# Kernel tuning notes

Measured on AMD Instinct MI355X. Metric: run time of the kernel, lower is better.

## Reference

```python
import jax, jax.numpy as jnp
import numpy as np

SEQ_LEN, BZ, D_IN = 512, 64, 1024
HIDDEN, D_OUT, NUM_LANG = 256, 1024, 16


def setup_inputs() -> dict:
    key = jax.random.key(0)
    ks = jax.random.split(key, 6)
    x = jax.random.normal(ks[0], (SEQ_LEN, BZ, D_IN), dtype=jnp.float32)
    lang_ids = jax.random.randint(ks[1], (BZ,), 0, NUM_LANG, dtype=jnp.int64)
    # Per-language 2-layer MLP params, stacked over the language axis.
    # Stored as [in, out] so y = x @ W + b (same math as torch Linear's x @ W.T + b).
    s1 = 1.0 / np.sqrt(D_IN)
    s2 = 1.0 / np.sqrt(HIDDEN)
    W1 = jax.random.uniform(ks[2], (NUM_LANG, D_IN, HIDDEN), jnp.float32, -s1, s1)
    b1 = jax.random.uniform(ks[3], (NUM_LANG, HIDDEN), jnp.float32, -s1, s1)
    W2 = jax.random.uniform(ks[4], (NUM_LANG, HIDDEN, D_OUT), jnp.float32, -s2, s2)
    b2 = jax.random.uniform(ks[5], (NUM_LANG, D_OUT), jnp.float32, -s2, s2)
    return {"x": x, "lang_ids": lang_ids, "W1": W1, "b1": b1, "W2": W2, "b2": b2}


def reference(x, lang_ids, W1, b1, W2, b2):
    # Gather each batch element's expert weights, then do batched GEMMs.
    # Equivalent to the torch loop (dispatch -> per-expert MLP -> combine),
    # without redundant gather/scatter passes.
    W1g = W1[lang_ids]            # [bz, d_in, hidden]
    b1g = b1[lang_ids]            # [bz, hidden]
    W2g = W2[lang_ids]            # [bz, hidden, d_out]
    b2g = b2[lang_ids]            # [bz, d_out]
    h = jnp.einsum('sbd,bdh->sbh', x, W1g) + b1g[None, :, :]
    h = jax.nn.relu(h)
    y = jnp.einsum('sbh,bho->sbo', h, W2g) + b2g[None, :, :]
    return y
```

## Files before the change

kernel.cpp:

```cpp
#include <hip/hip_runtime.h>

#define SEQ 512
#define BZ  64
#define DIN 1024
#define HID 256
#define DOUT 1024
#define NLANG 16

typedef __attribute__((ext_vector_type(8))) __bf16 bf16x8;
typedef __attribute__((ext_vector_type(4))) float f32x4;

__device__ __forceinline__ unsigned short f2bf(float f) {
    return __builtin_bit_cast(unsigned short, (__bf16)f);
}
__device__ __forceinline__ unsigned int f2bf_pack(float lo, float hi) {
    return (unsigned int)f2bf(lo) | ((unsigned int)f2bf(hi) << 16);
}

template<int K, int N>
__global__ __launch_bounds__(256)
void prep_frags(const float* __restrict__ src, unsigned short* __restrict__ dst) {
    constexpr int K32 = K / 32, N16 = N / 16;
    const int gid = blockIdx.x * 256 + threadIdx.x;
    const int l   = gid & 63;
    const int f   = gid >> 6;
    const int k32 = f & (K32 - 1);
    const int n16 = (f / K32) & (N16 - 1);
    const int lid = f / (K32 * N16);
    const float* s = src + ((long)lid * K + k32 * 32 + (l >> 4) * 8) * N + n16 * 16 + (l & 15);
    unsigned short o[8];
#pragma unroll
    for (int j = 0; j < 8; ++j) o[j] = f2bf(s[(long)j * N]);
    uint4 v;
    v.x = (unsigned int)o[0] | ((unsigned int)o[1] << 16);
    v.y = (unsigned int)o[2] | ((unsigned int)o[3] << 16);
    v.z = (unsigned int)o[4] | ((unsigned int)o[5] << 16);
    v.w = (unsigned int)o[6] | ((unsigned int)o[7] << 16);
    *(uint4*)(dst + (long)gid * 8) = v;
}

__global__ __launch_bounds__(256, 2)
void fused_mlp(const float* __restrict__ x,
               const unsigned short* __restrict__ W1f,
               const float* __restrict__ b1,
               const unsigned short* __restrict__ W2f,
               const float* __restrict__ b2,
               const int* __restrict__ lang,
               float* __restrict__ y) {
    __shared__ unsigned short sA[2][64 * 64];
    __shared__ unsigned short sH[64 * 256];

    const int b  = blockIdx.x;
    const int st = blockIdx.y;
    const int t  = threadIdx.x;
    const int l  = t & 63;
    const int w  = t >> 6;
    const int lid = lang[b];
    const int s0  = st * 64;
    const long xbase = (long)s0 * BZ * DIN + (long)b * DIN;

    const f32x4 z4 = {0.f, 0.f, 0.f, 0.f};

    f32x4 acc1[4][4];
#pragma unroll
    for (int mi = 0; mi < 4; ++mi)
#pragma unroll
        for (int ni = 0; ni < 4; ++ni) acc1[mi][ni] = z4;

    float4 xr[4];
#define LOADX(KT)                                                                 \
    {                                                                             \
        _Pragma("unroll")                                                         \
        for (int j = 0; j < 4; ++j) {                                             \
            int u = t + 256 * j, m = u >> 4, c4 = u & 15;                         \
            xr[j] = *(const float4*)(x + xbase + (long)m * (BZ * DIN) + (KT) * 64 + c4 * 4); \
        }                                                                         \
    }
#define WRITEX(BUF)                                                               \
    {                                                                             \
        char* cA = (char*)sA[BUF];                                                \
        _Pragma("unroll")                                                         \
        for (int j = 0; j < 4; ++j) {                                             \
            int u = t + 256 * j, m = u >> 4, c4 = u & 15;                         \
            uint2 p;                                                              \
            p.x = f2bf_pack(xr[j].x, xr[j].y);                                    \
            p.y = f2bf_pack(xr[j].z, xr[j].w);                                    \
            *(uint2*)(cA + (((m * 128) + c4 * 8) ^ ((m & 7) << 4))) = p;          \
        }                                                                         \
    }

    LOADX(0);
    WRITEX(0);
    __syncthreads();

    const unsigned short* w1p = W1f + (((long)lid * 16 + w * 4) * 32) * 512 + (long)l * 8;

    for (int kt = 0; kt < 16; ++kt) {
        const int cur = kt & 1;
        if (kt < 15) LOADX(kt + 1);

        bf16x8 bv[2][4];
#pragma unroll
        for (int ks = 0; ks < 2; ++ks)
#pragma unroll
            for (int ni = 0; ni < 4; ++ni)
                bv[ks][ni] = __builtin_bit_cast(bf16x8,
                    *(const uint4*)(w1p + (long)ni * 16384 + (kt * 2 + ks) * 512));

        char* cA = (char*)sA[cur];
#pragma unroll
        for (int ks = 0; ks < 2; ++ks) {
            bf16x8 av[4];
#pragma unroll
            for (int mi = 0; mi < 4; ++mi) {
                int row = mi * 16 + (l & 15);
                int ch  = ks * 4 + (l >> 4);
                av[mi] = __builtin_bit_cast(bf16x8,
                    *(const uint4*)(cA + row * 128 + ((ch ^ (row & 7)) << 4)));
            }
#pragma unroll
            for (int mi = 0; mi < 4; ++mi)
#pragma unroll
                for (int ni = 0; ni < 4; ++ni)
                    acc1[mi][ni] = __builtin_amdgcn_mfma_f32_16x16x32_bf16(
                        av[mi], bv[ks][ni], acc1[mi][ni], 0, 0, 0);
        }

        if (kt < 15) WRITEX(cur ^ 1);
        __syncthreads();
    }

    {
        float bvv[4];
#pragma unroll
        for (int ni = 0; ni < 4; ++ni)
            bvv[ni] = b1[lid * HID + w * 64 + ni * 16 + (l & 15)];
        char* cH = (char*)sH;
#pragma unroll
        for (int mi = 0; mi < 4; ++mi)
#pragma unroll
            for (int r = 0; r < 4; ++r) {
                int row = mi * 16 + (l >> 4) * 4 + r;
#pragma unroll
                for (int ni = 0; ni < 4; ++ni) {
                    int col = w * 64 + ni * 16 + (l & 15);
                    float v = acc1[mi][ni][r] + bvv[ni];
                    v = v > 0.f ? v : 0.f;
                    *(unsigned short*)(cH + row * 512 + (((col >> 3) ^ (row & 7)) << 4)
                                       + (col & 7) * 2) = f2bf(v);
                }
            }
    }
    __syncthreads();

    bf16x8 a2[4][8];
    {
        char* cH = (char*)sH;
#pragma unroll
        for (int mi = 0; mi < 4; ++mi)
#pragma unroll
            for (int ks = 0; ks < 8; ++ks) {
                int row = mi * 16 + (l & 15);
                int ch  = ks * 4 + (l >> 4);
                a2[mi][ks] = __builtin_bit_cast(bf16x8,
                    *(const uint4*)(cH + row * 512 + ((ch ^ (row & 7)) << 4)));
            }
    }

    const unsigned short* w2p = W2f + (((long)lid * 64 + w * 16) * 8) * 512 + (long)l * 8;

#pragma unroll 1
    for (int nc = 0; nc < 4; ++nc) {
        f32x4 acc[4][4];
#pragma unroll
        for (int mi = 0; mi < 4; ++mi)
#pragma unroll
            for (int ni = 0; ni < 4; ++ni) acc[mi][ni] = z4;

        const unsigned short* wp = w2p + (long)nc * 4 * 4096;

        bf16x8 pv[2][4];
#pragma unroll
        for (int ni = 0; ni < 4; ++ni)
            pv[0][ni] = __builtin_bit_cast(bf16x8, *(const uint4*)(wp + (long)ni * 4096));
#pragma unroll
        for (int ks = 0; ks < 8; ++ks) {
            const int cb = ks & 1;
            if (ks < 7) {
#pragma unroll
                for (int ni = 0; ni < 4; ++ni)
                    pv[cb ^ 1][ni] = __builtin_bit_cast(bf16x8,
                        *(const uint4*)(wp + (long)ni * 4096 + (ks + 1) * 512));
            }
#pragma unroll
            for (int mi = 0; mi < 4; ++mi)
#pragma unroll
                for (int ni = 0; ni < 4; ++ni)
                    acc[mi][ni] = __builtin_amdgcn_mfma_f32_16x16x32_bf16(
                        a2[mi][ks], pv[cb][ni], acc[mi][ni], 0, 0, 0);
        }

        float b2v[4];
#pragma unroll
        for (int ni = 0; ni < 4; ++ni)
            b2v[ni] = b2[lid * DOUT + w * 256 + nc * 64 + ni * 16 + (l & 15)];
#pragma unroll
        for (int mi = 0; mi < 4; ++mi)
#pragma unroll
            for (int r = 0; r < 4; ++r) {
                int row = mi * 16 + (l >> 4) * 4 + r;
#pragma unroll
                for (int ni = 0; ni < 4; ++ni) {
                    int col = w * 256 + nc * 64 + ni * 16 + (l & 15);
                    y[((long)(s0 + row) * BZ + b) * DOUT + col] = acc[mi][ni][r] + b2v[ni];
                }
            }
    }
#undef LOADX
#undef WRITEX
}

extern "C" void kernel_launch(void* const* d_in, const int* in_sizes, int n_in,
                              void* d_out, int out_size, void* d_ws, size_t ws_size,
                              hipStream_t stream) {
    const float* x    = (const float*)d_in[0];
    const int*   lang = (const int*)d_in[1];
    const float* W1   = (const float*)d_in[2];
    const float* b1   = (const float*)d_in[3];
    const float* W2   = (const float*)d_in[4];
    const float* b2   = (const float*)d_in[5];
    float* y = (float*)d_out;

    unsigned short* W1f = (unsigned short*)d_ws;
    unsigned short* W2f = (unsigned short*)((char*)d_ws + (size_t)NLANG * HID * DIN * 2);

    prep_frags<DIN, HID><<<2048, 256, 0, stream>>>(W1, W1f);
    prep_frags<HID, DOUT><<<2048, 256, 0, stream>>>(W2, W2f);

    fused_mlp<<<dim3(BZ, SEQ / 64), 256, 0, stream>>>(x, W1f, b1, W2f, b2, lang, y);
}
```

Baseline: 102.3 us.

## Halve sequence tile to 32 rows, raise occupancy, and software-pipeline weight loads

Each block now handles 32 sequence rows instead of 64, which doubles the grid and lets launch bounds target 4 blocks per SM with half the LDS and fewer accumulator registers. The first GEMM double-buffers W1 fragment loads per 32-wide k step. The second GEMM flattens into one fully unrolled 32-step loop that prefetches both the W2 fragments and the H fragments from LDS, replacing the held a2 register array. The intent is better latency hiding through occupancy and prefetch. The cost is that W1 and W2 are streamed twice as often per output row, which adds L2 traffic.

```diff
diff --git a/kernel.cpp b/kernel.cpp
--- a/kernel.cpp
+++ b/kernel.cpp
@@ -39,7 +39,7 @@
     *(uint4*)(dst + (long)gid * 8) = v;
 }
 
-__global__ __launch_bounds__(256, 2)
+__global__ __launch_bounds__(256, 4)
 void fused_mlp(const float* __restrict__ x,
                const unsigned short* __restrict__ W1f,
                const float* __restrict__ b1,
@@ -47,8 +47,8 @@
                const float* __restrict__ b2,
                const int* __restrict__ lang,
                float* __restrict__ y) {
-    __shared__ unsigned short sA[2][64 * 64];
-    __shared__ unsigned short sH[64 * 256];
+    __shared__ unsigned short sA[2][32 * 64];
+    __shared__ unsigned short sH[32 * 256];
 
     const int b  = blockIdx.x;
     const int st = blockIdx.y;
@@ -56,22 +56,22 @@
     const int l  = t & 63;
     const int w  = t >> 6;
     const int lid = lang[b];
-    const int s0  = st * 64;
+    const int s0  = st * 32;
     const long xbase = (long)s0 * BZ * DIN + (long)b * DIN;
 
     const f32x4 z4 = {0.f, 0.f, 0.f, 0.f};
 
-    f32x4 acc1[4][4];
-#pragma unroll
-    for (int mi = 0; mi < 4; ++mi)
+    f32x4 acc1[2][4];
+#pragma unroll
+    for (int mi = 0; mi < 2; ++mi)
 #pragma unroll
         for (int ni = 0; ni < 4; ++ni) acc1[mi][ni] = z4;
 
-    float4 xr[4];
+    float4 xr[2];
 #define LOADX(KT)                                                                 \
     {                                                                             \
         _Pragma("unroll")                                                         \
-        for (int j = 0; j < 4; ++j) {                                             \
+        for (int j = 0; j < 2; ++j) {                                             \
             int u = t + 256 * j, m = u >> 4, c4 = u & 15;                         \
             xr[j] = *(const float4*)(x + xbase + (long)m * (BZ * DIN) + (KT) * 64 + c4 * 4); \
         }                                                                         \
@@ -80,7 +80,7 @@
     {                                                                             \
         char* cA = (char*)sA[BUF];                                                \
         _Pragma("unroll")                                                         \
-        for (int j = 0; j < 4; ++j) {                                             \
+        for (int j = 0; j < 2; ++j) {                                             \
             int u = t + 256 * j, m = u >> 4, c4 = u & 15;                         \
             uint2 p;                                                              \
             p.x = f2bf_pack(xr[j].x, xr[j].y);                                    \
@@ -89,44 +89,45 @@
         }                                                                         \
     }
 
+    const unsigned short* w1p = W1f + (((long)lid * 16 + w * 4) * 32) * 512 + (long)l * 8;
+
     LOADX(0);
     WRITEX(0);
+    bf16x8 bvp[2][4];
+#pragma unroll
+    for (int ni = 0; ni < 4; ++ni)
+        bvp[0][ni] = __builtin_bit_cast(bf16x8, *(const uint4*)(w1p + (long)ni * 16384));
     __syncthreads();
 
-    const unsigned short* w1p = W1f + (((long)lid * 16 + w * 4) * 32) * 512 + (long)l * 8;
-
     for (int kt = 0; kt < 16; ++kt) {
-        const int cur = kt & 1;
         if (kt < 15) LOADX(kt + 1);
-
-        bf16x8 bv[2][4];
-#pragma unroll
-        for (int ks = 0; ks < 2; ++ks)
-#pragma unroll
-            for (int ni = 0; ni < 4; ++ni)
-                bv[ks][ni] = __builtin_bit_cast(bf16x8,
-                    *(const uint4*)(w1p + (long)ni * 16384 + (kt * 2 + ks) * 512));
-
-        char* cA = (char*)sA[cur];
+        char* cA = (char*)sA[kt & 1];
 #pragma unroll
         for (int ks = 0; ks < 2; ++ks) {
-            bf16x8 av[4];
-#pragma unroll
-            for (int mi = 0; mi < 4; ++mi) {
+            const int k32 = kt * 2 + ks;
+            const int cur = k32 & 1;
+            if (k32 < 31) {
+#pragma unroll
+                for (int ni = 0; ni < 4; ++ni)
+                    bvp[cur ^ 1][ni] = __builtin_bit_cast(bf16x8,
+                        *(const uint4*)(w1p + (long)ni * 16384 + (k32 + 1) * 512));
+            }
+            bf16x8 av[2];
+#pragma unroll
+            for (int mi = 0; mi < 2; ++mi) {
                 int row = mi * 16 + (l & 15);
                 int ch  = ks * 4 + (l >> 4);
                 av[mi] = __builtin_bit_cast(bf16x8,
                     *(const uint4*)(cA + row * 128 + ((ch ^ (row & 7)) << 4)));
             }
 #pragma unroll
-            for (int mi = 0; mi < 4; ++mi)
+            for (int mi = 0; mi < 2; ++mi)
 #pragma unroll
                 for (int ni = 0; ni < 4; ++ni)
                     acc1[mi][ni] = __builtin_amdgcn_mfma_f32_16x16x32_bf16(
-                        av[mi], bv[ks][ni], acc1[mi][ni], 0, 0, 0);
-        }
-
-        if (kt < 15) WRITEX(cur ^ 1);
+                        av[mi], bvp[cur][ni], acc1[mi][ni], 0, 0, 0);
+        }
+        if (kt < 15) WRITEX((kt & 1) ^ 1);
         __syncthreads();
     }
 
@@ -137,7 +138,7 @@
             bvv[ni] = b1[lid * HID + w * 64 + ni * 16 + (l & 15)];
         char* cH = (char*)sH;
 #pragma unroll
-        for (int mi = 0; mi < 4; ++mi)
+        for (int mi = 0; mi < 2; ++mi)
 #pragma unroll
             for (int r = 0; r < 4; ++r) {
                 int row = mi * 16 + (l >> 4) * 4 + r;
@@ -153,68 +154,72 @@
     }
     __syncthreads();
 
-    bf16x8 a2[4][8];
-    {
-        char* cH = (char*)sH;
-#pragma unroll
-        for (int mi = 0; mi < 4; ++mi)
-#pragma unroll
-            for (int ks = 0; ks < 8; ++ks) {
+    char* cH = (char*)sH;
+    const unsigned short* w2p = W2f + (((long)lid * 64 + w * 16) * 8) * 512 + (long)l * 8;
+
+    float b2v[4][4];
+#pragma unroll
+    for (int nc = 0; nc < 4; ++nc)
+#pragma unroll
+        for (int ni = 0; ni < 4; ++ni)
+            b2v[nc][ni] = b2[lid * DOUT + w * 256 + nc * 64 + ni * 16 + (l & 15)];
+
+    bf16x8 pv[2][4], av2[2][2];
+#pragma unroll
+    for (int ni = 0; ni < 4; ++ni)
+        pv[0][ni] = __builtin_bit_cast(bf16x8, *(const uint4*)(w2p + (long)ni * 4096));
+#pragma unroll
+    for (int mi = 0; mi < 2; ++mi) {
+        int row = mi * 16 + (l & 15);
+        int ch  = (l >> 4);
+        av2[0][mi] = __builtin_bit_cast(bf16x8,
+            *(const uint4*)(cH + row * 512 + ((ch ^ (row & 7)) << 4)));
+    }
+
+    f32x4 acc[2][4];
+#pragma unroll
+    for (int step = 0; step < 32; ++step) {
+        const int nc = step >> 3, ks = step & 7, cur = step & 1;
+        if (ks == 0) {
+#pragma unroll
+            for (int mi = 0; mi < 2; ++mi)
+#pragma unroll
+                for (int ni = 0; ni < 4; ++ni) acc[mi][ni] = z4;
+        }
+        if (step < 31) {
+            const int ns = step + 1, nnc = ns >> 3, nks = ns & 7;
+#pragma unroll
+            for (int ni = 0; ni < 4; ++ni)
+                pv[cur ^ 1][ni] = __builtin_bit_cast(bf16x8,
+                    *(const uint4*)(w2p + (long)(nnc * 4 + ni) * 4096 + nks * 512));
+#pragma unroll
+            for (int mi = 0; mi < 2; ++mi) {
                 int row = mi * 16 + (l & 15);
-                int ch  = ks * 4 + (l >> 4);
-                a2[mi][ks] = __builtin_bit_cast(bf16x8,
+                int ch  = nks * 4 + (l >> 4);
+                av2[cur ^ 1][mi] = __builtin_bit_cast(bf16x8,
                     *(const uint4*)(cH + row * 512 + ((ch ^ (row & 7)) << 4)));
             }
-    }
-
-    const unsigned short* w2p = W2f + (((long)lid * 64 + w * 16) * 8) * 512 + (long)l * 8;
-
-#pragma unroll 1
-    for (int nc = 0; nc < 4; ++nc) {
-        f32x4 acc[4][4];
-#pragma unroll
-        for (int mi = 0; mi < 4; ++mi)
-#pragma unroll
-            for (int ni = 0; ni < 4; ++ni) acc[mi][ni] = z4;
-
-        const unsigned short* wp = w2p + (long)nc * 4 * 4096;
-
-        bf16x8 pv[2][4];
-#pragma unroll
-        for (int ni = 0; ni < 4; ++ni)
-            pv[0][ni] = __builtin_bit_cast(bf16x8, *(const uint4*)(wp + (long)ni * 4096));
-#pragma unroll
-        for (int ks = 0; ks < 8; ++ks) {
-            const int cb = ks & 1;
-            if (ks < 7) {
-#pragma unroll
-                for (int ni = 0; ni < 4; ++ni)
-                    pv[cb ^ 1][ni] = __builtin_bit_cast(bf16x8,
-                        *(const uint4*)(wp + (long)ni * 4096 + (ks + 1) * 512));
-            }
-#pragma unroll
-            for (int mi = 0; mi < 4; ++mi)
-#pragma unroll
-                for (int ni = 0; ni < 4; ++ni)
-                    acc[mi][ni] = __builtin_amdgcn_mfma_f32_16x16x32_bf16(
-                        a2[mi][ks], pv[cb][ni], acc[mi][ni], 0, 0, 0);
-        }
-
-        float b2v[4];
-#pragma unroll
-        for (int ni = 0; ni < 4; ++ni)
-            b2v[ni] = b2[lid * DOUT + w * 256 + nc * 64 + ni * 16 + (l & 15)];
-#pragma unroll
-        for (int mi = 0; mi < 4; ++mi)
-#pragma unroll
-            for (int r = 0; r < 4; ++r) {
-                int row = mi * 16 + (l >> 4) * 4 + r;
-#pragma unroll
-                for (int ni = 0; ni < 4; ++ni) {
-                    int col = w * 256 + nc * 64 + ni * 16 + (l & 15);
-                    y[((long)(s0 + row) * BZ + b) * DOUT + col] = acc[mi][ni][r] + b2v[ni];
+        }
+#pragma unroll
+        for (int mi = 0; mi < 2; ++mi)
+#pragma unroll
+            for (int ni = 0; ni < 4; ++ni)
+                acc[mi][ni] = __builtin_amdgcn_mfma_f32_16x16x32_bf16(
+                    av2[cur][mi], pv[cur][ni], acc[mi][ni], 0, 0, 0);
+        if (ks == 7) {
+#pragma unroll
+            for (int mi = 0; mi < 2; ++mi)
+#pragma unroll
+                for (int r = 0; r < 4; ++r) {
+                    int row = mi * 16 + (l >> 4) * 4 + r;
+#pragma unroll
+                    for (int ni = 0; ni < 4; ++ni) {
+                        int col = w * 256 + nc * 64 + ni * 16 + (l & 15);
+                        y[((long)(s0 + row) * BZ + b) * DOUT + col] =
+                            acc[mi][ni][r] + b2v[nc][ni];
+                    }
                 }
-            }
+        }
     }
 #undef LOADX
 #undef WRITEX
@@ -237,5 +242,5 @@
     prep_frags<DIN, HID><<<2048, 256, 0, stream>>>(W1, W1f);
     prep_frags<HID, DOUT><<<2048, 256, 0, stream>>>(W2, W2f);
 
-    fused_mlp<<<dim3(BZ, SEQ / 64), 256, 0, stream>>>(x, W1f, b1, W2f, b2, lang, y);
-}
+    fused_mlp<<<dim3(BZ, SEQ / 32), 256, 0, stream>>>(x, W1f, b1, W2f, b2, lang, y);
+}
```

After: 127.4 us. 1.24x slower.

## Software-pipeline weight fragment loads with ring buffers, remap blocks, raise occupancy

Applied to the files above, without the earlier changes.

Replaces per-iteration weight loads in both GEMM phases with three-slot register ring buffers that prefetch two K-steps ahead. The second GEMM is fully unrolled, and the hidden-activation fragments are streamed from LDS two at a time instead of held in registers. __syncthreads is swapped for an explicit lgkmcnt wait plus s_barrier. The grid becomes 1D with a block-index remap, and launch bounds are raised to 3 blocks per CU. The goal is to hide global load latency and raise occupancy, at the cost of more register pressure, possible spills from the full unroll, and changed L2 locality.

```diff
diff --git a/kernel.cpp b/kernel.cpp
--- a/kernel.cpp
+++ b/kernel.cpp
@@ -9,6 +9,8 @@
 
 typedef __attribute__((ext_vector_type(8))) __bf16 bf16x8;
 typedef __attribute__((ext_vector_type(4))) float f32x4;
+
+#define LGKM0 asm volatile("s_waitcnt lgkmcnt(0)" ::: "memory")
 
 __device__ __forceinline__ unsigned short f2bf(float f) {
     return __builtin_bit_cast(unsigned short, (__bf16)f);
@@ -39,7 +41,7 @@
     *(uint4*)(dst + (long)gid * 8) = v;
 }
 
-__global__ __launch_bounds__(256, 2)
+__global__ __launch_bounds__(256, 3)
 void fused_mlp(const float* __restrict__ x,
                const unsigned short* __restrict__ W1f,
                const float* __restrict__ b1,
@@ -50,8 +52,11 @@
     __shared__ unsigned short sA[2][64 * 64];
     __shared__ unsigned short sH[64 * 256];
 
-    const int b  = blockIdx.x;
-    const int st = blockIdx.y;
+    const int n  = blockIdx.x;
+    const int v  = ((n & 7) << 6) | (n >> 3);
+    const int b  = v >> 3;
+    const int st = v & 7;
+
     const int t  = threadIdx.x;
     const int l  = t & 63;
     const int w  = t >> 6;
@@ -89,27 +94,38 @@
         }                                                                         \
     }
 
+    const unsigned short* w1p = W1f + (((long)lid * 16 + w * 4) * 32) * 512 + (long)l * 8;
+
+    float bvv[4];
+#pragma unroll
+    for (int ni = 0; ni < 4; ++ni)
+        bvv[ni] = b1[lid * HID + w * 64 + ni * 16 + (l & 15)];
+
     LOADX(0);
+    bf16x8 ring1[3][4];
+#pragma unroll
+    for (int s = 0; s < 2; ++s)
+#pragma unroll
+        for (int ni = 0; ni < 4; ++ni)
+            ring1[s][ni] = __builtin_bit_cast(bf16x8,
+                *(const uint4*)(w1p + (long)ni * 16384 + s * 512));
     WRITEX(0);
-    __syncthreads();
-
-    const unsigned short* w1p = W1f + (((long)lid * 16 + w * 4) * 32) * 512 + (long)l * 8;
-
+    LGKM0;
+    __builtin_amdgcn_s_barrier();
+
+#pragma unroll
     for (int kt = 0; kt < 16; ++kt) {
-        const int cur = kt & 1;
         if (kt < 15) LOADX(kt + 1);
-
-        bf16x8 bv[2][4];
-#pragma unroll
-        for (int ks = 0; ks < 2; ++ks)
-#pragma unroll
-            for (int ni = 0; ni < 4; ++ni)
-                bv[ks][ni] = __builtin_bit_cast(bf16x8,
-                    *(const uint4*)(w1p + (long)ni * 16384 + (kt * 2 + ks) * 512));
-
-        char* cA = (char*)sA[cur];
+        char* cA = (char*)sA[kt & 1];
 #pragma unroll
         for (int ks = 0; ks < 2; ++ks) {
+            const int k32 = kt * 2 + ks;
+            if (k32 < 30) {
+#pragma unroll
+                for (int ni = 0; ni < 4; ++ni)
+                    ring1[(k32 + 2) % 3][ni] = __builtin_bit_cast(bf16x8,
+                        *(const uint4*)(w1p + (long)ni * 16384 + (k32 + 2) * 512));
+            }
             bf16x8 av[4];
 #pragma unroll
             for (int mi = 0; mi < 4; ++mi) {
@@ -123,18 +139,16 @@
 #pragma unroll
                 for (int ni = 0; ni < 4; ++ni)
                     acc1[mi][ni] = __builtin_amdgcn_mfma_f32_16x16x32_bf16(
-                        av[mi], bv[ks][ni], acc1[mi][ni], 0, 0, 0);
-        }
-
-        if (kt < 15) WRITEX(cur ^ 1);
-        __syncthreads();
+                        av[mi], ring1[k32 % 3][ni], acc1[mi][ni], 0, 0, 0);
+        }
+        if (kt < 15) {
+            WRITEX((kt & 1) ^ 1);
+            LGKM0;
+            __builtin_amdgcn_s_barrier();
+        }
     }
 
     {
-        float bvv[4];
-#pragma unroll
-        for (int ni = 0; ni < 4; ++ni)
-            bvv[ni] = b1[lid * HID + w * 64 + ni * 16 + (l & 15)];
         char* cH = (char*)sH;
 #pragma unroll
         for (int mi = 0; mi < 4; ++mi)
@@ -144,77 +158,85 @@
 #pragma unroll
                 for (int ni = 0; ni < 4; ++ni) {
                     int col = w * 64 + ni * 16 + (l & 15);
-                    float v = acc1[mi][ni][r] + bvv[ni];
-                    v = v > 0.f ? v : 0.f;
+                    float vv = acc1[mi][ni][r] + bvv[ni];
+                    vv = vv > 0.f ? vv : 0.f;
                     *(unsigned short*)(cH + row * 512 + (((col >> 3) ^ (row & 7)) << 4)
-                                       + (col & 7) * 2) = f2bf(v);
+                                       + (col & 7) * 2) = f2bf(vv);
                 }
             }
     }
-    __syncthreads();
-
-    bf16x8 a2[4][8];
-    {
-        char* cH = (char*)sH;
+    LGKM0;
+    __builtin_amdgcn_s_barrier();
+
+    char* cH = (char*)sH;
+    const unsigned short* w2p = W2f + (((long)lid * 64 + w * 16) * 8) * 512 + (long)l * 8;
+
+    bf16x8 pv[3][4], av2[2][4];
+#pragma unroll
+    for (int s = 0; s < 2; ++s)
+#pragma unroll
+        for (int ni = 0; ni < 4; ++ni)
+            pv[s][ni] = __builtin_bit_cast(bf16x8,
+                *(const uint4*)(w2p + (long)ni * 4096 + s * 512));
+#pragma unroll
+    for (int mi = 0; mi < 4; ++mi) {
+        int row = mi * 16 + (l & 15);
+        int ch  = (l >> 4);
+        av2[0][mi] = __builtin_bit_cast(bf16x8,
+            *(const uint4*)(cH + row * 512 + ((ch ^ (row & 7)) << 4)));
+    }
+
+    f32x4 acc[4][4];
+    float b2v[4];
+#pragma unroll
+    for (int step = 0; step < 32; ++step) {
+        const int nc = step >> 3, ks = step & 7;
+        if (ks == 0) {
+#pragma unroll
+            for (int mi = 0; mi < 4; ++mi)
+#pragma unroll
+                for (int ni = 0; ni < 4; ++ni) acc[mi][ni] = z4;
+#pragma unroll
+            for (int ni = 0; ni < 4; ++ni)
+                b2v[ni] = b2[lid * DOUT + w * 256 + nc * 64 + ni * 16 + (l & 15)];
+        }
+        if (step < 30) {
+            const int s2 = step + 2, nc2 = s2 >> 3, ks2 = s2 & 7;
+#pragma unroll
+            for (int ni = 0; ni < 4; ++ni)
+                pv[s2 % 3][ni] = __builtin_bit_cast(bf16x8,
+                    *(const uint4*)(w2p + (long)(nc2 * 4 + ni) * 4096 + ks2 * 512));
+        }
+        if (step < 31) {
+            const int s1 = step + 1, ks1 = s1 & 7;
+#pragma unroll
+            for (int mi = 0; mi < 4; ++mi) {
+                int row = mi * 16 + (l & 15);
+                int ch  = ks1 * 4 + (l >> 4);
+                av2[s1 & 1][mi] = __builtin_bit_cast(bf16x8,
+                    *(const uint4*)(cH + row * 512 + ((ch ^ (row & 7)) << 4)));
+            }
+        }
 #pragma unroll
         for (int mi = 0; mi < 4; ++mi)
 #pragma unroll
-            for (int ks = 0; ks < 8; ++ks) {
-                int row = mi * 16 + (l & 15);
-                int ch  = ks * 4 + (l >> 4);
-                a2[mi][ks] = __builtin_bit_cast(bf16x8,
-                    *(const uint4*)(cH + row * 512 + ((ch ^ (row & 7)) << 4)));
-            }
-    }
-
-    const unsigned short* w2p = W2f + (((long)lid * 64 + w * 16) * 8) * 512 + (long)l * 8;
-
-#pragma unroll 1
-    for (int nc = 0; nc < 4; ++nc) {
-        f32x4 acc[4][4];
-#pragma unroll
-        for (int mi = 0; mi < 4; ++mi)
-#pragma unroll
-            for (int ni = 0; ni < 4; ++ni) acc[mi][ni] = z4;
-
-        const unsigned short* wp = w2p + (long)nc * 4 * 4096;
-
-        bf16x8 pv[2][4];
-#pragma unroll
-        for (int ni = 0; ni < 4; ++ni)
-            pv[0][ni] = __builtin_bit_cast(bf16x8, *(const uint4*)(wp + (long)ni * 4096));
-#pragma unroll
-        for (int ks = 0; ks < 8; ++ks) {
-            const int cb = ks & 1;
-            if (ks < 7) {
-#pragma unroll
-                for (int ni = 0; ni < 4; ++ni)
-                    pv[cb ^ 1][ni] = __builtin_bit_cast(bf16x8,
-                        *(const uint4*)(wp + (long)ni * 4096 + (ks + 1) * 512));
-            }
+            for (int ni = 0; ni < 4; ++ni)
+                acc[mi][ni] = __builtin_amdgcn_mfma_f32_16x16x32_bf16(
+                    av2[step & 1][mi], pv[step % 3][ni], acc[mi][ni], 0, 0, 0);
+        if (ks == 7) {
 #pragma unroll
             for (int mi = 0; mi < 4; ++mi)
 #pragma unroll
-                for (int ni = 0; ni < 4; ++ni)
-                    acc[mi][ni] = __builtin_amdgcn_mfma_f32_16x16x32_bf16(
-                        a2[mi][ks], pv[cb][ni], acc[mi][ni], 0, 0, 0);
-        }
-
-        float b2v[4];
-#pragma unroll
-        for (int ni = 0; ni < 4; ++ni)
-            b2v[ni] = b2[lid * DOUT + w * 256 + nc * 64 + ni * 16 + (l & 15)];
-#pragma unroll
-        for (int mi = 0; mi < 4; ++mi)
-#pragma unroll
-            for (int r = 0; r < 4; ++r) {
-                int row = mi * 16 + (l >> 4) * 4 + r;
-#pragma unroll
-                for (int ni = 0; ni < 4; ++ni) {
-                    int col = w * 256 + nc * 64 + ni * 16 + (l & 15);
-                    y[((long)(s0 + row) * BZ + b) * DOUT + col] = acc[mi][ni][r] + b2v[ni];
+                for (int r = 0; r < 4; ++r) {
+                    int row = mi * 16 + (l >> 4) * 4 + r;
+#pragma unroll
+                    for (int ni = 0; ni < 4; ++ni) {
+                        int col = w * 256 + nc * 64 + ni * 16 + (l & 15);
+                        y[((long)(s0 + row) * BZ + b) * DOUT + col] =
+                            acc[mi][ni][r] + b2v[ni];
+                    }
                 }
-            }
+        }
     }
 #undef LOADX
 #undef WRITEX
@@ -237,5 +259,5 @@
     prep_frags<DIN, HID><<<2048, 256, 0, stream>>>(W1, W1f);
     prep_frags<HID, DOUT><<<2048, 256, 0, stream>>>(W2, W2f);
 
-    fused_mlp<<<dim3(BZ, SEQ / 64), 256, 0, stream>>>(x, W1f, b1, W2f, b2, lang, y);
-}
+    fused_mlp<<<dim3(BZ * (SEQ / 64)), 256, 0, stream>>>(x, W1f, b1, W2f, b2, lang, y);
+}
```

Result: slower. 162.4 us (+58.7%).

## Use 512-thread blocks with wider x tiles and pipelined second GEMM

Applied to the files above, without the earlier changes.

Doubles the block size to 8 waves, so each wave covers half as many hidden and output columns in both GEMMs. The x tile is now loaded 256 columns at a time into a single 64x256 LDS buffer, which cuts the first GEMM to 4 outer steps. The second GEMM streams hidden fragments from LDS with double buffering instead of holding them all in registers. The aim is lower register pressure and more waves per CU to hide memory latency, at the cost of more barriers and no overlap between LDS writes and compute.

```diff
diff --git a/kernel.cpp b/kernel.cpp
--- a/kernel.cpp
+++ b/kernel.cpp
@@ -39,7 +39,7 @@
     *(uint4*)(dst + (long)gid * 8) = v;
 }
 
-__global__ __launch_bounds__(256, 2)
+__global__ __launch_bounds__(512, 4)
 void fused_mlp(const float* __restrict__ x,
                const unsigned short* __restrict__ W1f,
                const float* __restrict__ b1,
@@ -47,8 +47,10 @@
                const float* __restrict__ b2,
                const int* __restrict__ lang,
                float* __restrict__ y) {
-    __shared__ unsigned short sA[2][64 * 64];
+    __shared__ unsigned short sX[64 * 256];
     __shared__ unsigned short sH[64 * 256];
+    char* cX = (char*)sX;
+    char* cH = (char*)sH;
 
     const int b  = blockIdx.x;
     const int st = blockIdx.y;
@@ -57,164 +59,160 @@
     const int w  = t >> 6;
     const int lid = lang[b];
     const int s0  = st * 64;
-    const long xbase = (long)s0 * BZ * DIN + (long)b * DIN;
+    const long xstride = (long)BZ * DIN;
+    const float* xb = x + (long)s0 * xstride + (long)b * DIN;
 
     const f32x4 z4 = {0.f, 0.f, 0.f, 0.f};
 
-    f32x4 acc1[4][4];
+    f32x4 acc1[4][2];
 #pragma unroll
     for (int mi = 0; mi < 4; ++mi)
 #pragma unroll
-        for (int ni = 0; ni < 4; ++ni) acc1[mi][ni] = z4;
-
-    float4 xr[4];
-#define LOADX(KT)                                                                 \
-    {                                                                             \
-        _Pragma("unroll")                                                         \
-        for (int j = 0; j < 4; ++j) {                                             \
-            int u = t + 256 * j, m = u >> 4, c4 = u & 15;                         \
-            xr[j] = *(const float4*)(x + xbase + (long)m * (BZ * DIN) + (KT) * 64 + c4 * 4); \
-        }                                                                         \
-    }
-#define WRITEX(BUF)                                                               \
-    {                                                                             \
-        char* cA = (char*)sA[BUF];                                                \
-        _Pragma("unroll")                                                         \
-        for (int j = 0; j < 4; ++j) {                                             \
-            int u = t + 256 * j, m = u >> 4, c4 = u & 15;                         \
-            uint2 p;                                                              \
-            p.x = f2bf_pack(xr[j].x, xr[j].y);                                    \
-            p.y = f2bf_pack(xr[j].z, xr[j].w);                                    \
-            *(uint2*)(cA + (((m * 128) + c4 * 8) ^ ((m & 7) << 4))) = p;          \
-        }                                                                         \
-    }
+        for (int ni = 0; ni < 2; ++ni) acc1[mi][ni] = z4;
+
+    float4 xr[8];
+#define LOADX(KT)                                                                  \
+    {                                                                              \
+        _Pragma("unroll")                                                          \
+        for (int j = 0; j < 8; ++j)                                                \
+            xr[j] = *(const float4*)(xb + (long)(8 * j + w) * xstride + (KT) * 256 + l * 4); \
+    }
+#define WRITEX                                                                     \
+    {                                                                              \
+        _Pragma("unroll")                                                          \
+        for (int j = 0; j < 8; ++j) {                                              \
+            int row = 8 * j + w;                                                   \
+            int ch = l >> 1, half = l & 1;                                         \
+            uint2 p;                                                               \
+            p.x = f2bf_pack(xr[j].x, xr[j].y);                                     \
+            p.y = f2bf_pack(xr[j].z, xr[j].w);                                     \
+            *(uint2*)(cX + row * 512 + ((ch ^ (row & 7)) << 4) + half * 8) = p;    \
+        }                                                                          \
+    }
+
+    const unsigned short* w1p = W1f + (((long)lid * 16 + w * 2) * 32) * 512 + (long)l * 8;
+
+    float bvv[2];
+#pragma unroll
+    for (int ni = 0; ni < 2; ++ni)
+        bvv[ni] = b1[lid * HID + w * 32 + ni * 16 + (l & 15)];
 
     LOADX(0);
-    WRITEX(0);
-    __syncthreads();
-
-    const unsigned short* w1p = W1f + (((long)lid * 16 + w * 4) * 32) * 512 + (long)l * 8;
-
-    for (int kt = 0; kt < 16; ++kt) {
-        const int cur = kt & 1;
-        if (kt < 15) LOADX(kt + 1);
-
-        bf16x8 bv[2][4];
-#pragma unroll
-        for (int ks = 0; ks < 2; ++ks)
-#pragma unroll
-            for (int ni = 0; ni < 4; ++ni)
-                bv[ks][ni] = __builtin_bit_cast(bf16x8,
-                    *(const uint4*)(w1p + (long)ni * 16384 + (kt * 2 + ks) * 512));
-
-        char* cA = (char*)sA[cur];
-#pragma unroll
-        for (int ks = 0; ks < 2; ++ks) {
+    bf16x8 bvp[2][2];
+#pragma unroll
+    for (int ni = 0; ni < 2; ++ni)
+        bvp[0][ni] = __builtin_bit_cast(bf16x8, *(const uint4*)(w1p + (long)ni * 16384));
+
+#pragma unroll 1
+    for (int kt = 0; kt < 4; ++kt) {
+        WRITEX;
+        __syncthreads();
+        if (kt < 3) LOADX(kt + 1);
+#pragma unroll
+        for (int j = 0; j < 8; ++j) {
+            const int k32 = kt * 8 + j;
+            if (kt < 3 || j < 7) {
+#pragma unroll
+                for (int ni = 0; ni < 2; ++ni)
+                    bvp[(j + 1) & 1][ni] = __builtin_bit_cast(bf16x8,
+                        *(const uint4*)(w1p + (long)ni * 16384 + (k32 + 1) * 512));
+            }
             bf16x8 av[4];
 #pragma unroll
             for (int mi = 0; mi < 4; ++mi) {
                 int row = mi * 16 + (l & 15);
-                int ch  = ks * 4 + (l >> 4);
+                int ch  = j * 4 + (l >> 4);
                 av[mi] = __builtin_bit_cast(bf16x8,
-                    *(const uint4*)(cA + row * 128 + ((ch ^ (row & 7)) << 4)));
+                    *(const uint4*)(cX + row * 512 + ((ch ^ (row & 7)) << 4)));
             }
 #pragma unroll
             for (int mi = 0; mi < 4; ++mi)
 #pragma unroll
-                for (int ni = 0; ni < 4; ++ni)
+                for (int ni = 0; ni < 2; ++ni)
                     acc1[mi][ni] = __builtin_amdgcn_mfma_f32_16x16x32_bf16(
-                        av[mi], bv[ks][ni], acc1[mi][ni], 0, 0, 0);
-        }
-
-        if (kt < 15) WRITEX(cur ^ 1);
+                        av[mi], bvp[j & 1][ni], acc1[mi][ni], 0, 0, 0);
+        }
         __syncthreads();
     }
 
-    {
-        float bvv[4];
-#pragma unroll
-        for (int ni = 0; ni < 4; ++ni)
-            bvv[ni] = b1[lid * HID + w * 64 + ni * 16 + (l & 15)];
-        char* cH = (char*)sH;
+#pragma unroll
+    for (int mi = 0; mi < 4; ++mi)
+#pragma unroll
+        for (int r = 0; r < 4; ++r) {
+            int row = mi * 16 + (l >> 4) * 4 + r;
+#pragma unroll
+            for (int ni = 0; ni < 2; ++ni) {
+                int col = w * 32 + ni * 16 + (l & 15);
+                float v = acc1[mi][ni][r] + bvv[ni];
+                v = v > 0.f ? v : 0.f;
+                *(unsigned short*)(cH + row * 512 + (((col >> 3) ^ (row & 7)) << 4)
+                                   + (col & 7) * 2) = f2bf(v);
+            }
+        }
+    __syncthreads();
+
+    const unsigned short* w2p = W2f + (((long)lid * 64 + w * 8) * 8) * 512 + (long)l * 8;
+
+    bf16x8 pv[2][4], av2[2][4];
+#pragma unroll
+    for (int ni = 0; ni < 4; ++ni)
+        pv[0][ni] = __builtin_bit_cast(bf16x8, *(const uint4*)(w2p + (long)ni * 4096));
+#pragma unroll
+    for (int mi = 0; mi < 4; ++mi) {
+        int row = mi * 16 + (l & 15);
+        int ch  = (l >> 4);
+        av2[0][mi] = __builtin_bit_cast(bf16x8,
+            *(const uint4*)(cH + row * 512 + ((ch ^ (row & 7)) << 4)));
+    }
+
+    f32x4 acc[4][4];
+    float b2v[4];
+#pragma unroll
+    for (int s = 0; s < 16; ++s) {
+        const int nc = s >> 3, ks = s & 7, cur = s & 1;
+        if (ks == 0) {
+#pragma unroll
+            for (int mi = 0; mi < 4; ++mi)
+#pragma unroll
+                for (int ni = 0; ni < 4; ++ni) acc[mi][ni] = z4;
+#pragma unroll
+            for (int ni = 0; ni < 4; ++ni)
+                b2v[ni] = b2[lid * DOUT + w * 128 + nc * 64 + ni * 16 + (l & 15)];
+        }
+        if (s < 15) {
+            const int ns = s + 1, nq = (ns >> 3) * 4, ks1 = ns & 7;
+#pragma unroll
+            for (int ni = 0; ni < 4; ++ni)
+                pv[cur ^ 1][ni] = __builtin_bit_cast(bf16x8,
+                    *(const uint4*)(w2p + (long)(nq + ni) * 4096 + ks1 * 512));
+#pragma unroll
+            for (int mi = 0; mi < 4; ++mi) {
+                int row = mi * 16 + (l & 15);
+                int ch  = ks1 * 4 + (l >> 4);
+                av2[cur ^ 1][mi] = __builtin_bit_cast(bf16x8,
+                    *(const uint4*)(cH + row * 512 + ((ch ^ (row & 7)) << 4)));
+            }
+        }
 #pragma unroll
         for (int mi = 0; mi < 4; ++mi)
 #pragma unroll
-            for (int r = 0; r < 4; ++r) {
-                int row = mi * 16 + (l >> 4) * 4 + r;
-#pragma unroll
-                for (int ni = 0; ni < 4; ++ni) {
-                    int col = w * 64 + ni * 16 + (l & 15);
-                    float v = acc1[mi][ni][r] + bvv[ni];
-                    v = v > 0.f ? v : 0.f;
-                    *(unsigned short*)(cH + row * 512 + (((col >> 3) ^ (row & 7)) << 4)
-                                       + (col & 7) * 2) = f2bf(v);
+            for (int ni = 0; ni < 4; ++ni)
+                acc[mi][ni] = __builtin_amdgcn_mfma_f32_16x16x32_bf16(
+                    av2[cur][mi], pv[cur][ni], acc[mi][ni], 0, 0, 0);
+        if (ks == 7) {
+#pragma unroll
+            for (int mi = 0; mi < 4; ++mi)
+#pragma unroll
+                for (int r = 0; r < 4; ++r) {
+                    int row = mi * 16 + (l >> 4) * 4 + r;
+#pragma unroll
+                    for (int ni = 0; ni < 4; ++ni) {
+                        int col = w * 128 + nc * 64 + ni * 16 + (l & 15);
+                        y[((long)(s0 + row) * BZ + b) * DOUT + col] =
+                            acc[mi][ni][r] + b2v[ni];
+                    }
                 }
-            }
-    }
-    __syncthreads();
-
-    bf16x8 a2[4][8];
-    {
-        char* cH = (char*)sH;
-#pragma unroll
-        for (int mi = 0; mi < 4; ++mi)
-#pragma unroll
-            for (int ks = 0; ks < 8; ++ks) {
-                int row = mi * 16 + (l & 15);
-                int ch  = ks * 4 + (l >> 4);
-                a2[mi][ks] = __builtin_bit_cast(bf16x8,
-                    *(const uint4*)(cH + row * 512 + ((ch ^ (row & 7)) << 4)));
-            }
-    }
-
-    const unsigned short* w2p = W2f + (((long)lid * 64 + w * 16) * 8) * 512 + (long)l * 8;
-
-#pragma unroll 1
-    for (int nc = 0; nc < 4; ++nc) {
-        f32x4 acc[4][4];
-#pragma unroll
-        for (int mi = 0; mi < 4; ++mi)
-#pragma unroll
-            for (int ni = 0; ni < 4; ++ni) acc[mi][ni] = z4;
-
-        const unsigned short* wp = w2p + (long)nc * 4 * 4096;
-
-        bf16x8 pv[2][4];
-#pragma unroll
-        for (int ni = 0; ni < 4; ++ni)
-            pv[0][ni] = __builtin_bit_cast(bf16x8, *(const uint4*)(wp + (long)ni * 4096));
-#pragma unroll
-        for (int ks = 0; ks < 8; ++ks) {
-            const int cb = ks & 1;
-            if (ks < 7) {
-#pragma unroll
-                for (int ni = 0; ni < 4; ++ni)
-                    pv[cb ^ 1][ni] = __builtin_bit_cast(bf16x8,
-                        *(const uint4*)(wp + (long)ni * 4096 + (ks + 1) * 512));
-            }
-#pragma unroll
-            for (int mi = 0; mi < 4; ++mi)
-#pragma unroll
-                for (int ni = 0; ni < 4; ++ni)
-                    acc[mi][ni] = __builtin_amdgcn_mfma_f32_16x16x32_bf16(
-                        a2[mi][ks], pv[cb][ni], acc[mi][ni], 0, 0, 0);
-        }
-
-        float b2v[4];
-#pragma unroll
-        for (int ni = 0; ni < 4; ++ni)
-            b2v[ni] = b2[lid * DOUT + w * 256 + nc * 64 + ni * 16 + (l & 15)];
-#pragma unroll
-        for (int mi = 0; mi < 4; ++mi)
-#pragma unroll
-            for (int r = 0; r < 4; ++r) {
-                int row = mi * 16 + (l >> 4) * 4 + r;
-#pragma unroll
-                for (int ni = 0; ni < 4; ++ni) {
-                    int col = w * 256 + nc * 64 + ni * 16 + (l & 15);
-                    y[((long)(s0 + row) * BZ + b) * DOUT + col] = acc[mi][ni][r] + b2v[ni];
-                }
-            }
+        }
     }
 #undef LOADX
 #undef WRITEX
@@ -237,5 +235,5 @@
     prep_frags<DIN, HID><<<2048, 256, 0, stream>>>(W1, W1f);
     prep_frags<HID, DOUT><<<2048, 256, 0, stream>>>(W2, W2f);
 
-    fused_mlp<<<dim3(BZ, SEQ / 64), 256, 0, stream>>>(x, W1f, b1, W2f, b2, lang, y);
-}
+    fused_mlp<<<dim3(BZ, SEQ / 64), 512, 0, stream>>>(x, W1f, b1, W2f, b2, lang, y);
+}
```

Result: slower. 150.5 us (+47.0%).
